# Performance work log

Measured on AMD Instinct MI355X. Metric: run time of the kernel, lower is better.

## Reference

```python
import jax, jax.numpy as jnp
import numpy as np
from jax import lax

FIRE_RATE = 0.5
RNG_BASE = jax.random.key(42)


def _max_pool3(x):
    # 3x3 max pool, stride 1, SAME padding, over NCHW channel slice
    return lax.reduce_window(x, -jnp.inf, lax.max, (1, 1, 3, 3), (1, 1, 1, 1), 'SAME')


def _depthwise(x, k):
    c = x.shape[1]
    return lax.conv_general_dilated(
        x, k, window_strides=(1, 1), padding='SAME',
        feature_group_count=c, dimension_numbers=('NCHW', 'OIHW', 'NCHW'))


def setup_inputs() -> dict:
    key = jax.random.key(0)
    k1, k2, k3, k4, k5 = jax.random.split(key, 5)
    B, C, H, W, HID = 8, 16, 96, 96, 128
    x = jax.random.normal(k1, (B, C, H, W), dtype=jnp.float32)
    w1 = jax.random.normal(k2, (HID, 3 * C), dtype=jnp.float32) * 0.1
    b1 = jax.random.normal(k3, (HID,), dtype=jnp.float32) * 0.1
    w2 = jax.random.normal(k4, (C, HID), dtype=jnp.float32) * 0.05
    b2 = jax.random.normal(k5, (C,), dtype=jnp.float32) * 0.05
    return {'x': x, 'w1': w1, 'b1': b1, 'w2': w2, 'b2': b2, 'steps': 16}


def reference(x, w1, b1, w2, b2, steps):
    C = x.shape[1]
    sobel_x = jnp.array([[-1., 0., 1.], [-2., 0., 2.], [-1., 0., 1.]], jnp.float32) / 8.0
    sobel_y = sobel_x.T
    kx = jnp.broadcast_to(sobel_x, (C, 1, 3, 3))
    ky = jnp.broadcast_to(sobel_y, (C, 1, 3, 3))

    def step_fn(xc, i):
        pre_life = _max_pool3(xc[:, 3:4]) > 0.1
        # perception: [x, grad_x, grad_y] along channels -> (B, 3C, H, W)
        p = jnp.concatenate([xc, _depthwise(xc, kx), _depthwise(xc, ky)], axis=1)
        y = jax.nn.relu(jnp.einsum('bchw,oc->bohw', p, w1) + b1[None, :, None, None])
        update = jnp.einsum('bhcw,oh->bocw'.replace('h', 'k'), y, w2) if False else \
            jnp.einsum('bkhw,ok->bohw', y, w2) + b2[None, :, None, None]
        key_i = jax.random.fold_in(RNG_BASE, i)
        fire = (jax.random.uniform(key_i, (xc.shape[0], 1, xc.shape[2], xc.shape[3]))
                < FIRE_RATE).astype(xc.dtype)
        xn = xc + update * fire
        post_life = _max_pool3(xn[:, 3:4]) > 0.1
        life = (pre_life & post_life).astype(xc.dtype)
        xn = jnp.clip(xn * life, -10.0, 10.0)
        return xn, None

    x_out, _ = lax.scan(step_fn, x, jnp.arange(steps))
    return x_out
```

## Files before the change

### kernel.cpp

```cpp
#include <hip/hip_runtime.h>
#include <stdint.h>

#define BB 8
#define CC 16
#define HH 96
#define WW 96
#define HID 128
#define HW (HH*WW)
#define CHW (CC*HW)
#define NPIX (BB*HW)
#define STEPS 16

typedef short s16x8 __attribute__((ext_vector_type(8)));
typedef float f32x4 __attribute__((ext_vector_type(4)));

__device__ __host__ inline unsigned short bf16rne(float x) {
  union { float f; uint32_t u; } v; v.f = x;
  return (unsigned short)((v.u + 0x7fffu + ((v.u >> 16) & 1u)) >> 16);
}
__device__ __host__ inline float bf16f(unsigned short h) {
  union { uint32_t u; float f; } v; v.u = ((uint32_t)h) << 16; return v.f;
}

__host__ __device__ inline void threefry2x32(uint32_t k0, uint32_t k1,
                                             uint32_t x0, uint32_t x1,
                                             uint32_t& o0, uint32_t& o1) {
  const uint32_t ks2 = k0 ^ k1 ^ 0x1BD11BDAu;
  uint32_t v0 = x0 + k0, v1 = x1 + k1;
#define RL(v, r) (((v) << (r)) | ((v) >> (32 - (r))))
#define RND(r) { v0 += v1; v1 = RL(v1, r); v1 ^= v0; }
  RND(13) RND(15) RND(26) RND(6)   v0 += k1;  v1 += ks2 + 1u;
  RND(17) RND(29) RND(16) RND(24)  v0 += ks2; v1 += k0 + 2u;
  RND(13) RND(15) RND(26) RND(6)   v0 += k0;  v1 += k1 + 3u;
  RND(17) RND(29) RND(16) RND(24)  v0 += k1;  v1 += ks2 + 4u;
  RND(13) RND(15) RND(26) RND(6)   v0 += ks2; v1 += k0 + 5u;
#undef RND
#undef RL
  o0 = v0; o1 = v1;
}

__device__ inline float fire_val(uint32_t ka, uint32_t kb, uint32_t j) {
  uint32_t r0, r1;
  threefry2x32(ka, kb, 0u, j, r0, r1);
  return ((r0 ^ r1) & 0x80000000u) ? 0.0f : 1.0f;
}

__global__ void prep_w(const float* __restrict__ w1, const float* __restrict__ b1,
                       const float* __restrict__ w2,
                       unsigned short* __restrict__ w1fh, unsigned short* __restrict__ w1fl,
                       unsigned short* __restrict__ w2fh, unsigned short* __restrict__ w2fl) {
  int i = blockIdx.x * 256 + threadIdx.x;
  if (i < HID * 64) {
    int m = i >> 6, k = i & 63;
    float x = (k < 48) ? w1[m * 48 + k] : (k == 48 ? b1[m] : 0.f);
    int q = m >> 5, mp = (m >> 4) & 1, lm = m & 15;
    int kg = k >> 3, e = k & 7, ks = kg >> 2, lg = kg & 3;
    int dst = ((((q * 2 + mp) * 2 + ks) * 64) + lg * 16 + lm) * 8 + e;
    unsigned short hb = bf16rne(x);
    w1fh[dst] = hb; w1fl[dst] = bf16rne(x - bf16f(hb));
  } else if (i < HID * 64 + CC * HID) {
    int j = i - HID * 64;
    int m = j >> 7, k = j & 127;
    float x = w2[m * 128 + k];
    int kg = k >> 3, e = k & 7, ks = kg >> 2, lg = kg & 3;
    int dst = ((ks * 64) + lg * 16 + m) * 8 + e;
    unsigned short hb = bf16rne(x);
    w2fh[dst] = hb; w2fl[dst] = bf16rne(x - bf16f(hb));
  }
}

__global__ __launch_bounds__(256, 4) void ca_fused(
    const float* __restrict__ src, const float* __restrict__ plprev,
    const unsigned short* __restrict__ w1fh, const unsigned short* __restrict__ w1fl,
    const unsigned short* __restrict__ w2fh, const unsigned short* __restrict__ w2fl,
    const float* __restrict__ b2,
    float* __restrict__ rawout, float* __restrict__ plout,
    uint32_t ka, uint32_t kb, int apply_life)
{
  __shared__ __align__(16) unsigned char smem[33024];
  unsigned char* pfh   = smem;
  unsigned char* pfl   = smem + 8192;
  float* xt            = (float*)(smem + 16384);
  float* raw3          = (float*)(smem + 22784);
  float* life_l        = (float*)(smem + 23360);
  unsigned char* yfh   = smem;
  unsigned char* yfl   = smem + 16384;
  float* fire_lds      = (float*)(smem + 32768);

  const int tid  = threadIdx.x;
  const int lane = tid & 63;
  const int q    = __builtin_amdgcn_readfirstlane(tid >> 6);
  const int b    = blockIdx.x & 7;
  const int t    = blockIdx.x >> 3;
  const int h0   = (t / 12) * 8, w0 = (t % 12) * 8;
  const int py   = lane >> 3, px = lane & 7;
  const int h    = h0 + py, w = w0 + px;
  const int P    = b * HW + h * WW + w;
  const int lm   = lane & 15, lg = lane >> 4;

  s16x8 a1h[2][2], a1l[2][2];
#pragma unroll
  for (int mp = 0; mp < 2; ++mp)
#pragma unroll
    for (int ks = 0; ks < 2; ++ks) {
      const int off = ((((q * 2 + mp) * 2 + ks) * 64) + lane) * 8;
      a1h[mp][ks] = *reinterpret_cast<const s16x8*>(w1fh + off);
      a1l[mp][ks] = *reinterpret_cast<const s16x8*>(w1fl + off);
    }
  const f32x4 b2v = reinterpret_cast<const f32x4*>(b2)[lg];

  float r3v = 0.f;
  if (apply_life && tid < 144) {
    const int r = tid / 12, c = tid - r * 12;
    const int hh = h0 - 2 + r, ww = w0 - 2 + c;
    if (hh >= 0 && hh < HH && ww >= 0 && ww < WW)
      r3v = src[b * CHW + 3 * HW + hh * WW + ww];
  }
  float plv = 0.f;
  if (apply_life && tid < 100) {
    const int r = tid / 10, c = tid - r * 10;
    const int hh = h0 - 1 + r, ww = w0 - 1 + c;
    if (hh >= 0 && hh < HH && ww >= 0 && ww < WW)
      plv = plprev[b * HW + hh * WW + ww];
  }
  float xreg[7];
#pragma unroll
  for (int ii = 0; ii < 7; ++ii) {
    xreg[ii] = 0.f;
    const int idx = tid + ii * 256;
    if (idx < CC * 100) {
      const int ch = idx / 100, rc = idx - ch * 100;
      const int r = rc / 10, c = rc - r * 10;
      const int hh = h0 - 1 + r, ww = w0 - 1 + c;
      if (hh >= 0 && hh < HH && ww >= 0 && ww < WW)
        xreg[ii] = src[b * CHW + ch * HW + hh * WW + ww];
    }
  }

  if (q == 0) fire_lds[lane] = fire_val(ka, kb, (uint32_t)P);

  if (apply_life) {
    if (tid < 144) raw3[tid] = r3v;
    __syncthreads();
    if (tid < 100) {
      const int r = tid / 10, c = tid - r * 10;
      float m = raw3[r * 12 + c];
      m = fmaxf(m, raw3[r * 12 + c + 1]); m = fmaxf(m, raw3[r * 12 + c + 2]);
      m = fmaxf(m, raw3[(r + 1) * 12 + c]);     m = fmaxf(m, raw3[(r + 1) * 12 + c + 1]);
      m = fmaxf(m, raw3[(r + 1) * 12 + c + 2]); m = fmaxf(m, raw3[(r + 2) * 12 + c]);
      m = fmaxf(m, raw3[(r + 2) * 12 + c + 1]); m = fmaxf(m, raw3[(r + 2) * 12 + c + 2]);
      life_l[tid] = ((m > 0.1f) && (plv > 0.1f)) ? 1.f : 0.f;
    }
    __syncthreads();
  }

#pragma unroll
  for (int ii = 0; ii < 7; ++ii) {
    const int idx = tid + ii * 256;
    if (idx < CC * 100) {
      const int ch = idx / 100, rc = idx - ch * 100;
      float v = xreg[ii];
      if (apply_life) {
        v *= life_l[rc];
        v = fminf(fmaxf(v, -10.f), 10.f);
      }
      xt[ch * 100 + rc] = v;
    }
  }
  __syncthreads();

  if (q == 0) {
    const int c0 = py * 10 + px;
    const float* x3 = xt + 3 * 100;
    float m = x3[c0];
    m = fmaxf(m, x3[c0 + 1]);  m = fmaxf(m, x3[c0 + 2]);
    m = fmaxf(m, x3[c0 + 10]); m = fmaxf(m, x3[c0 + 11]);
    m = fmaxf(m, x3[c0 + 12]); m = fmaxf(m, x3[c0 + 20]);
    m = fmaxf(m, x3[c0 + 21]); m = fmaxf(m, x3[c0 + 22]);
    plout[P] = m;
  }

  const int ctr = (1 + py) * 10 + (1 + px);
#define PUTP(K, X) do {                                                        \
    const int kg_ = (K) >> 3, e_ = (K) & 7;                                    \
    const int un_ = kg_ * 64 + ((lane + kg_) & 63);                            \
    const unsigned short hb_ = bf16rne(X);                                     \
    *reinterpret_cast<unsigned short*>(pfh + un_ * 16 + e_ * 2) = hb_;         \
    *reinterpret_cast<unsigned short*>(pfl + un_ * 16 + e_ * 2) =              \
        bf16rne((X) - bf16f(hb_));                                             \
  } while (0)
#pragma unroll
  for (int cc = 0; cc < 4; ++cc) {
    const int c = q + cc * 4;
    const float* xc = xt + c * 100;
    const float v00 = xc[ctr - 11], v01 = xc[ctr - 10], v02 = xc[ctr - 9];
    const float v10 = xc[ctr - 1],  v11 = xc[ctr],      v12 = xc[ctr + 1];
    const float v20 = xc[ctr + 9],  v21 = xc[ctr + 10], v22 = xc[ctr + 11];
    const float gx = ((v02 - v00) + 2.f * (v12 - v10) + (v22 - v20)) * 0.125f;
    const float gy = ((v20 - v00) + 2.f * (v21 - v01) + (v22 - v02)) * 0.125f;
    PUTP(c, v11);
    PUTP(16 + c, gx);
    PUTP(32 + c, gy);
  }
#undef PUTP
  {
    const int u6 = 6 * 64 + ((lane + 6) & 63);
    const int u7 = 7 * 64 + ((lane + 7) & 63);
    *reinterpret_cast<uint4*>(pfh + u6 * 16) = make_uint4(0x3f80u, 0u, 0u, 0u);
    *reinterpret_cast<uint4*>(pfl + u6 * 16) = make_uint4(0u, 0u, 0u, 0u);
    *reinterpret_cast<uint4*>(pfh + u7 * 16) = make_uint4(0u, 0u, 0u, 0u);
    *reinterpret_cast<uint4*>(pfl + u7 * 16) = make_uint4(0u, 0u, 0u, 0u);
  }
  __syncthreads();

  const int opx = q * 16 + lm;
  const int opy = opx >> 3, owx = opx & 7;
  const int octr = (1 + opy) * 10 + (1 + owx);
  float xcv[4];
#pragma unroll
  for (int r = 0; r < 4; ++r) xcv[r] = xt[(lg * 4 + r) * 100 + octr];

  f32x4 acc[2][4];
#pragma unroll
  for (int mp = 0; mp < 2; ++mp)
#pragma unroll
    for (int nt = 0; nt < 4; ++nt) acc[mp][nt] = (f32x4){0.f, 0.f, 0.f, 0.f};

#pragma unroll
  for (int nt = 0; nt < 4; ++nt) {
#pragma unroll
    for (int ks = 0; ks < 2; ++ks) {
      const int kg = ks * 4 + lg;
      const int un = kg * 64 + ((nt * 16 + lm + kg) & 63);
      const s16x8 bh = *reinterpret_cast<const s16x8*>(pfh + un * 16);
      const s16x8 bl = *reinterpret_cast<const s16x8*>(pfl + un * 16);
#pragma unroll
      for (int mp = 0; mp < 2; ++mp) {
        acc[mp][nt] = __builtin_amdgcn_mfma_f32_16x16x32_bf16(a1l[mp][ks], bh, acc[mp][nt], 0, 0, 0);
        acc[mp][nt] = __builtin_amdgcn_mfma_f32_16x16x32_bf16(a1h[mp][ks], bl, acc[mp][nt], 0, 0, 0);
        acc[mp][nt] = __builtin_amdgcn_mfma_f32_16x16x32_bf16(a1h[mp][ks], bh, acc[mp][nt], 0, 0, 0);
      }
    }
  }
  __syncthreads();

#pragma unroll
  for (int mp = 0; mp < 2; ++mp) {
    const int k0 = (2 * q + mp) * 16 + lg * 4;
    const int kg = k0 >> 3, e0 = k0 & 7;
#pragma unroll
    for (int nt = 0; nt < 4; ++nt) {
      const int un = kg * 64 + ((nt * 16 + lm + kg) & 63);
      unsigned int hwv[2], lwv[2];
#pragma unroll
      for (int pr = 0; pr < 2; ++pr) {
        const float ya = fmaxf(acc[mp][nt][2 * pr], 0.f);
        const float yb = fmaxf(acc[mp][nt][2 * pr + 1], 0.f);
        const unsigned short ha = bf16rne(ya), hb2 = bf16rne(yb);
        const unsigned short la = bf16rne(ya - bf16f(ha));
        const unsigned short lb = bf16rne(yb - bf16f(hb2));
        hwv[pr] = (unsigned int)ha | ((unsigned int)hb2 << 16);
        lwv[pr] = (unsigned int)la | ((unsigned int)lb << 16);
      }
      *reinterpret_cast<uint2*>(yfh + un * 16 + e0 * 2) = make_uint2(hwv[0], hwv[1]);
      *reinterpret_cast<uint2*>(yfl + un * 16 + e0 * 2) = make_uint2(lwv[0], lwv[1]);
    }
  }
  __syncthreads();

  f32x4 acc2 = (f32x4){0.f, 0.f, 0.f, 0.f};
#pragma unroll
  for (int ks = 0; ks < 4; ++ks) {
    const int woff = ((ks * 64) + lane) * 8;
    const s16x8 a2l = *reinterpret_cast<const s16x8*>(w2fl + woff);
    const s16x8 a2h = *reinterpret_cast<const s16x8*>(w2fh + woff);
    const int kg = ks * 4 + lg;
    const int un = kg * 64 + ((q * 16 + lm + kg) & 63);
    const s16x8 bh = *reinterpret_cast<const s16x8*>(yfh + un * 16);
    const s16x8 bl = *reinterpret_cast<const s16x8*>(yfl + un * 16);
    acc2 = __builtin_amdgcn_mfma_f32_16x16x32_bf16(a2l, bh, acc2, 0, 0, 0);
    acc2 = __builtin_amdgcn_mfma_f32_16x16x32_bf16(a2h, bl, acc2, 0, 0, 0);
    acc2 = __builtin_amdgcn_mfma_f32_16x16x32_bf16(a2h, bh, acc2, 0, 0, 0);
  }

  const float fire = fire_lds[opx];
  const int gb = b * CHW + (h0 + opy) * WW + (w0 + owx);
#pragma unroll
  for (int r = 0; r < 4; ++r) {
    const int c = lg * 4 + r;
    rawout[gb + c * HW] = xcv[r] + (acc2[r] + b2v[r]) * fire;
  }
}

__global__ __launch_bounds__(256) void ca_life(
    const float* __restrict__ prelife, const float* __restrict__ raw,
    float* __restrict__ xnext)
{
  const int lane = threadIdx.x & 63;
  const int g    = threadIdx.x >> 6;
  const int b    = blockIdx.x & 7;
  const int seg  = blockIdx.x >> 3;
  const int rem  = seg * 64 + lane;
  const int h = rem / WW;
  const int w = rem - h * WW;
  const int P = b * HW + rem;
  const bool hm = (h > 0), hp = (h < HH - 1), wm = (w > 0), wp = (w < WW - 1);

  float m2;
  {
    const float* xr = raw + b * CHW + 3 * HW + h * WW + w;
    m2 = xr[0];
    if (hm) {
      m2 = fmaxf(m2, xr[-WW]);
      if (wm) m2 = fmaxf(m2, xr[-WW - 1]);
      if (wp) m2 = fmaxf(m2, xr[-WW + 1]);
    }
    if (wm) m2 = fmaxf(m2, xr[-1]);
    if (wp) m2 = fmaxf(m2, xr[ 1]);
    if (hp) {
      m2 = fmaxf(m2, xr[WW]);
      if (wm) m2 = fmaxf(m2, xr[WW - 1]);
      if (wp) m2 = fmaxf(m2, xr[WW + 1]);
    }
  }
  const float life = ((prelife[P] > 0.1f) && (m2 > 0.1f)) ? 1.f : 0.f;

  const int base = b * CHW + h * WW + w;
#pragma unroll
  for (int cc = 0; cc < 4; ++cc) {
    const int c = g + cc * 4;
    float v = raw[base + c * HW] * life;
    v = fminf(fmaxf(v, -10.f), 10.f);
    xnext[base + c * HW] = v;
  }
}

extern "C" void kernel_launch(void* const* d_in, const int* in_sizes, int n_in,
                              void* d_out, int out_size, void* d_ws, size_t ws_size,
                              hipStream_t stream) {
  const float* x  = (const float*)d_in[0];
  const float* w1 = (const float*)d_in[1];
  const float* b1 = (const float*)d_in[2];
  const float* w2 = (const float*)d_in[3];
  const float* b2 = (const float*)d_in[4];
  float* out = (float*)d_out;

  char* ws = (char*)d_ws;
  const size_t BUF = (size_t)NPIX * CC * sizeof(float);
  float* rawA = (float*)(ws);
  float* rawB = (float*)(ws + BUF);
  float* plA  = (float*)(ws + 2 * BUF);
  float* plB  = (float*)(ws + 2 * BUF + (size_t)NPIX * 4);
  unsigned short* w1fh = (unsigned short*)(ws + 2 * BUF + 2 * (size_t)NPIX * 4);
  unsigned short* w1fl = w1fh + HID * 64;
  unsigned short* w2fh = w1fl + HID * 64;
  unsigned short* w2fl = w2fh + CC * HID;

  hipLaunchKernelGGL(prep_w, dim3(40), dim3(256), 0, stream,
                     w1, b1, w2, w1fh, w1fl, w2fh, w2fl);

  for (int i = 0; i < STEPS; ++i) {
    uint32_t ka, kb;
    threefry2x32(0u, 42u, 0u, (uint32_t)i, ka, kb);
    const float* src = (i == 0) ? x : ((i & 1) ? rawA : rawB);
    const float* plp = (i & 1) ? plA : plB;
    float* ro        = (i & 1) ? rawB : rawA;
    float* po        = (i & 1) ? plB : plA;
    hipLaunchKernelGGL(ca_fused, dim3(NPIX / 64), dim3(256), 0, stream,
                       src, plp, w1fh, w1fl, w2fh, w2fl, b2, ro, po,
                       ka, kb, (i == 0) ? 0 : 1);
  }
  hipLaunchKernelGGL(ca_life, dim3(NPIX / 64), dim3(256), 0, stream,
                     plB, rawB, out);
  (void)in_sizes; (void)n_in; (void)out_size; (void)ws_size;
}
```

Before: 227.4 us.

## Enlarge fused CA tile to 8x16 pixels processed in two MLP halves

Each block now covers an 8x16 pixel tile instead of 8x8, loading a shared 10x18 halo once and running the MLP twice over 64-pixel halves. This cuts the relative halo reload and life-mask overhead and halves the grid. The first-layer K layout is permuted so each wave writes its 16 perception features as whole vectors instead of scattered shorts. The trade-off is more LDS and registers per block, with occupancy lowered to 3 blocks and extra barriers inside the loop.

```diff
diff --git a/kernel.cpp b/kernel.cpp
--- a/kernel.cpp
+++ b/kernel.cpp
@@ -51,11 +51,20 @@
                        unsigned short* __restrict__ w2fh, unsigned short* __restrict__ w2fl) {
   int i = blockIdx.x * 256 + threadIdx.x;
   if (i < HID * 64) {
-    int m = i >> 6, k = i & 63;
-    float x = (k < 48) ? w1[m * 48 + k] : (k == 48 ? b1[m] : 0.f);
-    int q = m >> 5, mp = (m >> 4) & 1, lm = m & 15;
-    int kg = k >> 3, e = k & 7, ks = kg >> 2, lg = kg & 3;
-    int dst = ((((q * 2 + mp) * 2 + ks) * 64) + lg * 16 + lm) * 8 + e;
+    int m = i >> 6, kn = i & 63;
+    int q = kn >> 4, mm = kn & 15;
+    float x;
+    if (mm < 12) {
+      int cc = mm / 3, j = mm - cc * 3;
+      x = w1[m * 48 + j * 16 + q + cc * 4];
+    } else if (kn == 15) {
+      x = b1[m];
+    } else {
+      x = 0.f;
+    }
+    int mq = m >> 5, mp = (m >> 4) & 1, lm = m & 15;
+    int kg = kn >> 3, e = kn & 7, ks = kg >> 2, lg = kg & 3;
+    int dst = ((((mq * 2 + mp) * 2 + ks) * 64) + lg * 16 + lm) * 8 + e;
     unsigned short hb = bf16rne(x);
     w1fh[dst] = hb; w1fl[dst] = bf16rne(x - bf16f(hb));
   } else if (i < HID * 64 + CC * HID) {
@@ -69,7 +78,7 @@
   }
 }
 
-__global__ __launch_bounds__(256, 4) void ca_fused(
+__global__ __launch_bounds__(256, 3) void ca_fused(
     const float* __restrict__ src, const float* __restrict__ plprev,
     const unsigned short* __restrict__ w1fh, const unsigned short* __restrict__ w1fl,
     const unsigned short* __restrict__ w2fh, const unsigned short* __restrict__ w2fl,
@@ -77,25 +86,22 @@
     float* __restrict__ rawout, float* __restrict__ plout,
     uint32_t ka, uint32_t kb, int apply_life)
 {
-  __shared__ __align__(16) unsigned char smem[33024];
+  __shared__ __align__(16) unsigned char smem[46592];
   unsigned char* pfh   = smem;
   unsigned char* pfl   = smem + 8192;
-  float* xt            = (float*)(smem + 16384);
-  float* raw3          = (float*)(smem + 22784);
-  float* life_l        = (float*)(smem + 23360);
   unsigned char* yfh   = smem;
   unsigned char* yfl   = smem + 16384;
-  float* fire_lds      = (float*)(smem + 32768);
+  float* xt            = (float*)(smem + 32768);
+  float* raw3          = (float*)(smem + 44288);
+  float* life_l        = (float*)(smem + 45248);
+  float* fire_lds      = (float*)(smem + 45968);
 
   const int tid  = threadIdx.x;
   const int lane = tid & 63;
   const int q    = __builtin_amdgcn_readfirstlane(tid >> 6);
   const int b    = blockIdx.x & 7;
   const int t    = blockIdx.x >> 3;
-  const int h0   = (t / 12) * 8, w0 = (t % 12) * 8;
-  const int py   = lane >> 3, px = lane & 7;
-  const int h    = h0 + py, w = w0 + px;
-  const int P    = b * HW + h * WW + w;
+  const int h0   = (t / 6) * 8, w0 = (t % 6) * 16;
   const int lm   = lane & 15, lg = lane >> 4;
 
   s16x8 a1h[2][2], a1l[2][2];
@@ -110,185 +116,202 @@
   const f32x4 b2v = reinterpret_cast<const f32x4*>(b2)[lg];
 
   float r3v = 0.f;
-  if (apply_life && tid < 144) {
-    const int r = tid / 12, c = tid - r * 12;
+  if (apply_life && tid < 240) {
+    const int r = tid / 20, c = tid - r * 20;
     const int hh = h0 - 2 + r, ww = w0 - 2 + c;
     if (hh >= 0 && hh < HH && ww >= 0 && ww < WW)
       r3v = src[b * CHW + 3 * HW + hh * WW + ww];
   }
   float plv = 0.f;
-  if (apply_life && tid < 100) {
-    const int r = tid / 10, c = tid - r * 10;
+  if (apply_life && tid < 180) {
+    const int r = tid / 18, c = tid - r * 18;
     const int hh = h0 - 1 + r, ww = w0 - 1 + c;
     if (hh >= 0 && hh < HH && ww >= 0 && ww < WW)
       plv = plprev[b * HW + hh * WW + ww];
   }
-  float xreg[7];
-#pragma unroll
-  for (int ii = 0; ii < 7; ++ii) {
+  float xreg[12];
+#pragma unroll
+  for (int ii = 0; ii < 12; ++ii) {
     xreg[ii] = 0.f;
     const int idx = tid + ii * 256;
-    if (idx < CC * 100) {
-      const int ch = idx / 100, rc = idx - ch * 100;
-      const int r = rc / 10, c = rc - r * 10;
+    if (idx < CC * 180) {
+      const int ch = idx / 180, rc = idx - ch * 180;
+      const int r = rc / 18, c = rc - r * 18;
       const int hh = h0 - 1 + r, ww = w0 - 1 + c;
       if (hh >= 0 && hh < HH && ww >= 0 && ww < WW)
         xreg[ii] = src[b * CHW + ch * HW + hh * WW + ww];
     }
   }
 
-  if (q == 0) fire_lds[lane] = fire_val(ka, kb, (uint32_t)P);
-
   if (apply_life) {
-    if (tid < 144) raw3[tid] = r3v;
-    __syncthreads();
-    if (tid < 100) {
-      const int r = tid / 10, c = tid - r * 10;
-      float m = raw3[r * 12 + c];
-      m = fmaxf(m, raw3[r * 12 + c + 1]); m = fmaxf(m, raw3[r * 12 + c + 2]);
-      m = fmaxf(m, raw3[(r + 1) * 12 + c]);     m = fmaxf(m, raw3[(r + 1) * 12 + c + 1]);
-      m = fmaxf(m, raw3[(r + 1) * 12 + c + 2]); m = fmaxf(m, raw3[(r + 2) * 12 + c]);
-      m = fmaxf(m, raw3[(r + 2) * 12 + c + 1]); m = fmaxf(m, raw3[(r + 2) * 12 + c + 2]);
+    if (tid < 240) raw3[tid] = r3v;
+    __syncthreads();
+    if (tid < 180) {
+      const int r = tid / 18, c = tid - r * 18;
+      float m = fmaxf(fmaxf(raw3[r * 20 + c],        raw3[r * 20 + c + 1]),
+                      fmaxf(raw3[r * 20 + c + 2],    raw3[(r + 1) * 20 + c]));
+      m = fmaxf(m, fmaxf(raw3[(r + 1) * 20 + c + 1], raw3[(r + 1) * 20 + c + 2]));
+      m = fmaxf(m, fmaxf(raw3[(r + 2) * 20 + c],     raw3[(r + 2) * 20 + c + 1]));
+      m = fmaxf(m, raw3[(r + 2) * 20 + c + 2]);
       life_l[tid] = ((m > 0.1f) && (plv > 0.1f)) ? 1.f : 0.f;
     }
     __syncthreads();
   }
 
 #pragma unroll
-  for (int ii = 0; ii < 7; ++ii) {
+  for (int ii = 0; ii < 12; ++ii) {
     const int idx = tid + ii * 256;
-    if (idx < CC * 100) {
-      const int ch = idx / 100, rc = idx - ch * 100;
+    if (idx < CC * 180) {
+      const int ch = idx / 180, rc = idx - ch * 180;
       float v = xreg[ii];
       if (apply_life) {
         v *= life_l[rc];
         v = fminf(fmaxf(v, -10.f), 10.f);
       }
-      xt[ch * 100 + rc] = v;
+      xt[ch * 180 + rc] = v;
     }
   }
   __syncthreads();
 
-  if (q == 0) {
-    const int c0 = py * 10 + px;
-    const float* x3 = xt + 3 * 100;
-    float m = x3[c0];
-    m = fmaxf(m, x3[c0 + 1]);  m = fmaxf(m, x3[c0 + 2]);
-    m = fmaxf(m, x3[c0 + 10]); m = fmaxf(m, x3[c0 + 11]);
-    m = fmaxf(m, x3[c0 + 12]); m = fmaxf(m, x3[c0 + 20]);
-    m = fmaxf(m, x3[c0 + 21]); m = fmaxf(m, x3[c0 + 22]);
-    plout[P] = m;
-  }
-
-  const int ctr = (1 + py) * 10 + (1 + px);
-#define PUTP(K, X) do {                                                        \
-    const int kg_ = (K) >> 3, e_ = (K) & 7;                                    \
-    const int un_ = kg_ * 64 + ((lane + kg_) & 63);                            \
-    const unsigned short hb_ = bf16rne(X);                                     \
-    *reinterpret_cast<unsigned short*>(pfh + un_ * 16 + e_ * 2) = hb_;         \
-    *reinterpret_cast<unsigned short*>(pfl + un_ * 16 + e_ * 2) =              \
-        bf16rne((X) - bf16f(hb_));                                             \
-  } while (0)
-#pragma unroll
-  for (int cc = 0; cc < 4; ++cc) {
-    const int c = q + cc * 4;
-    const float* xc = xt + c * 100;
-    const float v00 = xc[ctr - 11], v01 = xc[ctr - 10], v02 = xc[ctr - 9];
-    const float v10 = xc[ctr - 1],  v11 = xc[ctr],      v12 = xc[ctr + 1];
-    const float v20 = xc[ctr + 9],  v21 = xc[ctr + 10], v22 = xc[ctr + 11];
-    const float gx = ((v02 - v00) + 2.f * (v12 - v10) + (v22 - v20)) * 0.125f;
-    const float gy = ((v20 - v00) + 2.f * (v21 - v01) + (v22 - v02)) * 0.125f;
-    PUTP(c, v11);
-    PUTP(16 + c, gx);
-    PUTP(32 + c, gy);
-  }
-#undef PUTP
-  {
-    const int u6 = 6 * 64 + ((lane + 6) & 63);
-    const int u7 = 7 * 64 + ((lane + 7) & 63);
-    *reinterpret_cast<uint4*>(pfh + u6 * 16) = make_uint4(0x3f80u, 0u, 0u, 0u);
-    *reinterpret_cast<uint4*>(pfl + u6 * 16) = make_uint4(0u, 0u, 0u, 0u);
-    *reinterpret_cast<uint4*>(pfh + u7 * 16) = make_uint4(0u, 0u, 0u, 0u);
-    *reinterpret_cast<uint4*>(pfl + u7 * 16) = make_uint4(0u, 0u, 0u, 0u);
-  }
-  __syncthreads();
-
-  const int opx = q * 16 + lm;
-  const int opy = opx >> 3, owx = opx & 7;
-  const int octr = (1 + opy) * 10 + (1 + owx);
-  float xcv[4];
-#pragma unroll
-  for (int r = 0; r < 4; ++r) xcv[r] = xt[(lg * 4 + r) * 100 + octr];
-
-  f32x4 acc[2][4];
-#pragma unroll
-  for (int mp = 0; mp < 2; ++mp)
-#pragma unroll
-    for (int nt = 0; nt < 4; ++nt) acc[mp][nt] = (f32x4){0.f, 0.f, 0.f, 0.f};
-
-#pragma unroll
-  for (int nt = 0; nt < 4; ++nt) {
-#pragma unroll
-    for (int ks = 0; ks < 2; ++ks) {
+  if (tid < 128) {
+    const int py = tid >> 4, pxx = tid & 15;
+    const float* x3 = xt + 3 * 180;
+    const int base = py * 18 + pxx;
+    float m = fmaxf(fmaxf(x3[base],      x3[base + 1]),
+                    fmaxf(x3[base + 2],  x3[base + 18]));
+    m = fmaxf(m, fmaxf(x3[base + 19], x3[base + 20]));
+    m = fmaxf(m, fmaxf(x3[base + 36], x3[base + 37]));
+    m = fmaxf(m, x3[base + 38]);
+    plout[b * HW + (h0 + py) * WW + w0 + pxx] = m;
+  } else {
+    const int i = tid - 128;
+    const int py = i >> 4, pxx = i & 15;
+    fire_lds[i] = fire_val(ka, kb, (uint32_t)(b * HW + (h0 + py) * WW + w0 + pxx));
+  }
+
+#pragma unroll 1
+  for (int hf = 0; hf < 2; ++hf) {
+    {
+      const int pp  = hf * 64 + lane;
+      const int ctr = ((pp >> 4) + 1) * 18 + (pp & 15) + 1;
+      float fv[12];
+#pragma unroll
+      for (int cc = 0; cc < 4; ++cc) {
+        const int c = q + cc * 4;
+        const float* xc = xt + c * 180;
+        const float v00 = xc[ctr - 19], v01 = xc[ctr - 18], v02 = xc[ctr - 17];
+        const float v10 = xc[ctr - 1],  v11 = xc[ctr],      v12 = xc[ctr + 1];
+        const float v20 = xc[ctr + 17], v21 = xc[ctr + 18], v22 = xc[ctr + 19];
+        fv[cc * 3 + 0] = v11;
+        fv[cc * 3 + 1] = ((v02 - v00) + 2.f * (v12 - v10) + (v22 - v20)) * 0.125f;
+        fv[cc * 3 + 2] = ((v20 - v00) + 2.f * (v21 - v01) + (v22 - v02)) * 0.125f;
+      }
+      s16x8 ph[2], pl[2];
+#pragma unroll
+      for (int u = 0; u < 2; ++u)
+#pragma unroll
+        for (int e = 0; e < 8; ++e) {
+          const int m = u * 8 + e;
+          if (m < 12) {
+            const unsigned short hb = bf16rne(fv[m]);
+            ph[u][e] = (short)hb;
+            pl[u][e] = (short)bf16rne(fv[m] - bf16f(hb));
+          } else if (m == 15) {
+            ph[u][e] = (short)((q == 0) ? 0x3F80 : 0);
+            pl[u][e] = 0;
+          } else {
+            ph[u][e] = 0; pl[u][e] = 0;
+          }
+        }
+#pragma unroll
+      for (int u = 0; u < 2; ++u) {
+        const int kgw = 2 * q + u;
+        const int un = kgw * 64 + ((lane + kgw) & 63);
+        *reinterpret_cast<s16x8*>(pfh + un * 16) = ph[u];
+        *reinterpret_cast<s16x8*>(pfl + un * 16) = pl[u];
+      }
+    }
+    __syncthreads();
+
+    const int opx = q * 16 + lm;
+    const int pp2 = hf * 64 + opx;
+    const int opy = pp2 >> 4, owx = pp2 & 15;
+    const int octr = (1 + opy) * 18 + (1 + owx);
+    float xcv[4];
+#pragma unroll
+    for (int r = 0; r < 4; ++r) xcv[r] = xt[(lg * 4 + r) * 180 + octr];
+
+    f32x4 acc[2][4];
+#pragma unroll
+    for (int mp = 0; mp < 2; ++mp)
+#pragma unroll
+      for (int nt = 0; nt < 4; ++nt) acc[mp][nt] = (f32x4){0.f, 0.f, 0.f, 0.f};
+
+#pragma unroll
+    for (int nt = 0; nt < 4; ++nt) {
+#pragma unroll
+      for (int ks = 0; ks < 2; ++ks) {
+        const int kg = ks * 4 + lg;
+        const int un = kg * 64 + ((nt * 16 + lm + kg) & 63);
+        const s16x8 bh = *reinterpret_cast<const s16x8*>(pfh + un * 16);
+        const s16x8 bl = *reinterpret_cast<const s16x8*>(pfl + un * 16);
+#pragma unroll
+        for (int mp = 0; mp < 2; ++mp) {
+          acc[mp][nt] = __builtin_amdgcn_mfma_f32_16x16x32_bf16(a1l[mp][ks], bh, acc[mp][nt], 0, 0, 0);
+          acc[mp][nt] = __builtin_amdgcn_mfma_f32_16x16x32_bf16(a1h[mp][ks], bl, acc[mp][nt], 0, 0, 0);
+          acc[mp][nt] = __builtin_amdgcn_mfma_f32_16x16x32_bf16(a1h[mp][ks], bh, acc[mp][nt], 0, 0, 0);
+        }
+      }
+    }
+    __syncthreads();
+
+#pragma unroll
+    for (int mp = 0; mp < 2; ++mp) {
+      const int k0 = (2 * q + mp) * 16 + lg * 4;
+      const int kg = k0 >> 3, e0 = k0 & 7;
+#pragma unroll
+      for (int nt = 0; nt < 4; ++nt) {
+        const int un = kg * 64 + ((nt * 16 + lm + kg) & 63);
+        unsigned int hwv[2], lwv[2];
+#pragma unroll
+        for (int pr = 0; pr < 2; ++pr) {
+          const float ya = fmaxf(acc[mp][nt][2 * pr], 0.f);
+          const float yb = fmaxf(acc[mp][nt][2 * pr + 1], 0.f);
+          const unsigned short ha = bf16rne(ya), hb2 = bf16rne(yb);
+          const unsigned short la = bf16rne(ya - bf16f(ha));
+          const unsigned short lb = bf16rne(yb - bf16f(hb2));
+          hwv[pr] = (unsigned int)ha | ((unsigned int)hb2 << 16);
+          lwv[pr] = (unsigned int)la | ((unsigned int)lb << 16);
+        }
+        *reinterpret_cast<uint2*>(yfh + un * 16 + e0 * 2) = make_uint2(hwv[0], hwv[1]);
+        *reinterpret_cast<uint2*>(yfl + un * 16 + e0 * 2) = make_uint2(lwv[0], lwv[1]);
+      }
+    }
+    __syncthreads();
+
+    f32x4 acc2 = (f32x4){0.f, 0.f, 0.f, 0.f};
+#pragma unroll
+    for (int ks = 0; ks < 4; ++ks) {
+      const int woff = ((ks * 64) + lane) * 8;
+      const s16x8 a2l = *reinterpret_cast<const s16x8*>(w2fl + woff);
+      const s16x8 a2h = *reinterpret_cast<const s16x8*>(w2fh + woff);
       const int kg = ks * 4 + lg;
-      const int un = kg * 64 + ((nt * 16 + lm + kg) & 63);
-      const s16x8 bh = *reinterpret_cast<const s16x8*>(pfh + un * 16);
-      const s16x8 bl = *reinterpret_cast<const s16x8*>(pfl + un * 16);
-#pragma unroll
-      for (int mp = 0; mp < 2; ++mp) {
-        acc[mp][nt] = __builtin_amdgcn_mfma_f32_16x16x32_bf16(a1l[mp][ks], bh, acc[mp][nt], 0, 0, 0);
-        acc[mp][nt] = __builtin_amdgcn_mfma_f32_16x16x32_bf16(a1h[mp][ks], bl, acc[mp][nt], 0, 0, 0);
-        acc[mp][nt] = __builtin_amdgcn_mfma_f32_16x16x32_bf16(a1h[mp][ks], bh, acc[mp][nt], 0, 0, 0);
-      }
-    }
-  }
-  __syncthreads();
-
-#pragma unroll
-  for (int mp = 0; mp < 2; ++mp) {
-    const int k0 = (2 * q + mp) * 16 + lg * 4;
-    const int kg = k0 >> 3, e0 = k0 & 7;
-#pragma unroll
-    for (int nt = 0; nt < 4; ++nt) {
-      const int un = kg * 64 + ((nt * 16 + lm + kg) & 63);
-      unsigned int hwv[2], lwv[2];
-#pragma unroll
-      for (int pr = 0; pr < 2; ++pr) {
-        const float ya = fmaxf(acc[mp][nt][2 * pr], 0.f);
-        const float yb = fmaxf(acc[mp][nt][2 * pr + 1], 0.f);
-        const unsigned short ha = bf16rne(ya), hb2 = bf16rne(yb);
-        const unsigned short la = bf16rne(ya - bf16f(ha));
-        const unsigned short lb = bf16rne(yb - bf16f(hb2));
-        hwv[pr] = (unsigned int)ha | ((unsigned int)hb2 << 16);
-        lwv[pr] = (unsigned int)la | ((unsigned int)lb << 16);
-      }
-      *reinterpret_cast<uint2*>(yfh + un * 16 + e0 * 2) = make_uint2(hwv[0], hwv[1]);
-      *reinterpret_cast<uint2*>(yfl + un * 16 + e0 * 2) = make_uint2(lwv[0], lwv[1]);
-    }
-  }
-  __syncthreads();
-
-  f32x4 acc2 = (f32x4){0.f, 0.f, 0.f, 0.f};
-#pragma unroll
-  for (int ks = 0; ks < 4; ++ks) {
-    const int woff = ((ks * 64) + lane) * 8;
-    const s16x8 a2l = *reinterpret_cast<const s16x8*>(w2fl + woff);
-    const s16x8 a2h = *reinterpret_cast<const s16x8*>(w2fh + woff);
-    const int kg = ks * 4 + lg;
-    const int un = kg * 64 + ((q * 16 + lm + kg) & 63);
-    const s16x8 bh = *reinterpret_cast<const s16x8*>(yfh + un * 16);
-    const s16x8 bl = *reinterpret_cast<const s16x8*>(yfl + un * 16);
-    acc2 = __builtin_amdgcn_mfma_f32_16x16x32_bf16(a2l, bh, acc2, 0, 0, 0);
-    acc2 = __builtin_amdgcn_mfma_f32_16x16x32_bf16(a2h, bl, acc2, 0, 0, 0);
-    acc2 = __builtin_amdgcn_mfma_f32_16x16x32_bf16(a2h, bh, acc2, 0, 0, 0);
-  }
-
-  const float fire = fire_lds[opx];
-  const int gb = b * CHW + (h0 + opy) * WW + (w0 + owx);
-#pragma unroll
-  for (int r = 0; r < 4; ++r) {
-    const int c = lg * 4 + r;
-    rawout[gb + c * HW] = xcv[r] + (acc2[r] + b2v[r]) * fire;
+      const int un = kg * 64 + ((q * 16 + lm + kg) & 63);
+      const s16x8 bh = *reinterpret_cast<const s16x8*>(yfh + un * 16);
+      const s16x8 bl = *reinterpret_cast<const s16x8*>(yfl + un * 16);
+      acc2 = __builtin_amdgcn_mfma_f32_16x16x32_bf16(a2l, bh, acc2, 0, 0, 0);
+      acc2 = __builtin_amdgcn_mfma_f32_16x16x32_bf16(a2h, bl, acc2, 0, 0, 0);
+      acc2 = __builtin_amdgcn_mfma_f32_16x16x32_bf16(a2h, bh, acc2, 0, 0, 0);
+    }
+
+    const float fire = fire_lds[pp2];
+    const int gb = b * CHW + (h0 + opy) * WW + (w0 + owx);
+#pragma unroll
+    for (int r = 0; r < 4; ++r) {
+      const int c = lg * 4 + r;
+      rawout[gb + c * HW] = xcv[r] + (acc2[r] + b2v[r]) * fire;
+    }
+    if (hf == 0) __syncthreads();
   }
 }
 
@@ -366,7 +389,7 @@
     const float* plp = (i & 1) ? plA : plB;
     float* ro        = (i & 1) ? rawB : rawA;
     float* po        = (i & 1) ? plB : plA;
-    hipLaunchKernelGGL(ca_fused, dim3(NPIX / 64), dim3(256), 0, stream,
+    hipLaunchKernelGGL(ca_fused, dim3(8 * 72), dim3(256), 0, stream,
                        src, plp, w1fh, w1fl, w2fh, w2fl, b2, ro, po,
                        ka, kb, (i == 0) ? 0 : 1);
   }
```

Measured after the change: 228.0 us. No clear change (+0.3%).
